# Performance work log

Measured on AMD Instinct MI355X. Metric: run time of the kernel, lower is better.

The kernel has to match this reference:

```python
import jax, jax.numpy as jnp
import numpy as np

WS = 8          # window_size
NH = 8          # num_heads
VD = 512        # values_dim
CD = 128        # coords_dim
INNER = 512     # inner_ratio * values_dim
E = INNER // NH # head_dim = 64
B, Hh, Ww_ = 2, 224, 224

# relative position indices (static)
_idx = np.array([[x, y] for x in range(WS) for y in range(WS)])
_rel = _idx[None, :, :] - _idx[:, None, :] + WS - 1  # (WS^2, WS^2, 2)
REL0 = jnp.asarray(_rel[:, :, 0])
REL1 = jnp.asarray(_rel[:, :, 1])

# shifted-window masks (static)
_s = WS * (WS // 2)
_rm = np.zeros((WS * WS, WS * WS), np.float32)
_rm[-_s:, :-_s] = -np.inf
_rm[:-_s, -_s:] = -np.inf
_cm = _rm.reshape(WS, WS, WS, WS).transpose(1, 0, 3, 2).reshape(WS * WS, WS * WS)
ROW_MASK = jnp.asarray(_rm)
COL_MASK = jnp.asarray(_cm)


def _rmsnorm(x, g, eps=1e-6):
    return x * g * jax.lax.rsqrt(jnp.mean(x * x, axis=-1, keepdims=True) + eps)


def _to_windows(x, b, Wh, Ww):
    # x: (b, hp, wp, INNER) with channel layout (e H) (head fastest)
    x = x.reshape(b, Wh, WS, Ww, WS, E, NH)
    return x.transpose(0, 6, 1, 3, 2, 4, 5).reshape(b, NH, Wh, Ww, WS * WS, E)


def setup_inputs() -> dict:
    key = jax.random.key(0)
    ks = jax.random.split(key, 8)
    s = 0.02
    return {
        "embedded_values": jax.random.normal(ks[0], (B, Hh, Ww_, VD), jnp.float32),
        "embedded_coords": jax.random.normal(ks[1], (B, Hh, Ww_, CD), jnp.float32),
        "Wqk_v": jax.random.normal(ks[2], (VD, 2 * INNER), jnp.float32) * s,
        "bqk_v": jnp.zeros((2 * INNER,), jnp.float32),
        "g_v": jnp.ones((2 * INNER,), jnp.float32),
        "Wv": jax.random.normal(ks[3], (VD, INNER), jnp.float32) * s,
        "bv": jnp.zeros((INNER,), jnp.float32),
        "Wqk_c": jax.random.normal(ks[4], (CD, 2 * INNER), jnp.float32) * s,
        "bqk_c": jnp.zeros((2 * INNER,), jnp.float32),
        "g_c": jnp.ones((2 * INNER,), jnp.float32),
        "pos_emb": jax.random.normal(ks[5], (2 * WS - 1, 2 * WS - 1), jnp.float32),
        "Wout": jax.random.normal(ks[6], (INNER, VD), jnp.float32) * s,
        "bout": jnp.zeros((VD,), jnp.float32),
    }


def reference(embedded_values, embedded_coords, Wqk_v, bqk_v, g_v, Wv, bv,
              Wqk_c, bqk_c, g_c, pos_emb, Wout, bout):
    b, h, w, _ = embedded_values.shape
    # projections; torch concat then rearrange '(d k)' k=3 interleaves channels -> reshape (..., INNER, 3)
    vqk = _rmsnorm(embedded_values @ Wqk_v + bqk_v, g_v)          # (b,h,w,2*INNER)
    vval = embedded_values @ Wv + bv                               # (b,h,w,INNER)
    v = jnp.concatenate([vqk, vval], axis=-1).reshape(b, h, w, INNER, 3)
    c = _rmsnorm(embedded_coords @ Wqk_c + bqk_c, g_c).reshape(b, h, w, INNER, 2)

    pad_h = (-h) % WS
    pad_w = (-w) % WS
    v = jnp.pad(v, ((0, 0), (0, pad_h), (0, pad_w), (0, 0), (0, 0)))
    c = jnp.pad(c, ((0, 0), (0, pad_h), (0, pad_w), (0, 0), (0, 0)))
    # shifted=True: roll windows by half window (no inverse roll in original)
    v = jnp.roll(v, (-(WS // 2), -(WS // 2)), axis=(1, 2))
    c = jnp.roll(c, (-(WS // 2), -(WS // 2)), axis=(1, 2))

    hp, wp = h + pad_h, w + pad_w
    Wh, Ww = hp // WS, wp // WS
    qv = _to_windows(v[..., 0], b, Wh, Ww)
    kv = _to_windows(v[..., 1], b, Wh, Ww)
    vv = _to_windows(v[..., 2], b, Wh, Ww)
    qc = _to_windows(c[..., 0], b, Wh, Ww)
    kc = _to_windows(c[..., 1], b, Wh, Ww)

    scale = float(E) ** 0.5
    dots = (jnp.einsum('bhijpe,bhijqe->bhijpq', qv, kv)
            + jnp.einsum('bhijpe,bhijqe->bhijpq', qc, kc)) / scale
    dots = dots + pos_emb[REL0, REL1]
    # shifted-window masks on last window row / column
    dots = dots.at[:, :, -1, :].add(ROW_MASK)
    dots = dots.at[:, :, :, -1].add(COL_MASK)

    attn = jax.nn.softmax(dots, axis=-1)
    y = jnp.einsum('bhijpq,bhijqe->bhijpe', attn, vv)
    # un-window; output channel layout is (H e) (head slow)
    y = y.reshape(b, NH, Wh, Ww, WS, WS, E).transpose(0, 2, 4, 3, 5, 1, 6)
    y = y.reshape(b, hp, wp, INNER)[:, :h, :w, :]
    return y @ Wout + bout
```

## Files before the change

kernel.cpp:

```cpp
#include <hip/hip_runtime.h>


using u16 = unsigned short;
typedef short bf16x8 __attribute__((ext_vector_type(8)));
typedef float f32x4 __attribute__((ext_vector_type(4)));
typedef u16 u16x4 __attribute__((ext_vector_type(4)));
typedef u16 u16x8 __attribute__((ext_vector_type(8)));

__device__ __forceinline__ float bf2f(u16 v) {
  return __uint_as_float(((unsigned)v) << 16);
}
__device__ __forceinline__ u16 f2bf(float f) {
  unsigned u = __float_as_uint(f);
  u += 0x7fffu + ((u >> 16) & 1u);
  return (u16)(u >> 16);
}

__device__ __forceinline__ void gld16(const u16* g, u16* l) {
  __builtin_amdgcn_global_load_lds(
      (const __attribute__((address_space(1))) unsigned*)g,
      (__attribute__((address_space(3))) unsigned*)l, 16, 0, 0);
}

__global__ void conv_bf16(const float* __restrict__ in, u16* __restrict__ out) {
  size_t i = ((size_t)blockIdx.x * 256 + threadIdx.x) * 8;
  float4 a = *(const float4*)(in + i);
  float4 b = *(const float4*)(in + i + 4);
  u16x8 o;
  o[0] = f2bf(a.x); o[1] = f2bf(a.y); o[2] = f2bf(a.z); o[3] = f2bf(a.w);
  o[4] = f2bf(b.x); o[5] = f2bf(b.y); o[6] = f2bf(b.z); o[7] = f2bf(b.w);
  *(u16x8*)(out + i) = o;
}

__global__ void prep_wv(const float* __restrict__ Wqkv, const float* __restrict__ Wv,
                        u16* __restrict__ out) {
  int idx = blockIdx.x * 256 + threadIdx.x;
  if (idx >= 1536 * 512) return;
  int j = idx >> 9, kk = idx & 511;
  int t = j >> 9, rr = j & 511, nn = rr >> 6, e = rr & 63;
  int cc = 3 * (e * 8 + nn) + t;
  float v = (cc < 1024) ? Wqkv[kk * 1024 + cc] : Wv[kk * 512 + (cc - 1024)];
  out[idx] = f2bf(v);
}

__global__ void prep_wc(const float* __restrict__ W, u16* __restrict__ out) {
  int idx = blockIdx.x * 256 + threadIdx.x;
  if (idx >= 1024 * 128) return;
  int j = idx >> 7, kk = idx & 127;
  int t = j >> 9, rr = j & 511, nn = rr >> 6, e = rr & 63;
  int cc = 2 * (e * 8 + nn) + t;
  out[idx] = f2bf(W[kk * 1024 + cc]);
}

__global__ void prep_wout(const float* __restrict__ W, u16* __restrict__ out) {
  int idx = blockIdx.x * 256 + threadIdx.x;
  if (idx >= 512 * 512) return;
  int o = idx >> 9, kk = idx & 511;
  out[idx] = f2bf(W[kk * 512 + o]);
}

__global__ void prep_vec(const float* __restrict__ bqkv, const float* __restrict__ g_v,
                         const float* __restrict__ bv, const float* __restrict__ bqkc,
                         const float* __restrict__ g_c,
                         float* __restrict__ bpv, float* __restrict__ gAv, float* __restrict__ gBv,
                         float* __restrict__ bpc, float* __restrict__ gAc, float* __restrict__ gBc) {
  int j = blockIdx.x * 256 + threadIdx.x;
  if (j < 1536) {
    int t = j >> 9, rr = j & 511, nn = rr >> 6, e = rr & 63;
    int cc = 3 * (e * 8 + nn) + t;
    if (cc < 1024) { bpv[j] = bqkv[cc]; gAv[j] = g_v[cc]; gBv[j] = 0.f; }
    else           { bpv[j] = bv[cc - 1024]; gAv[j] = 0.f; gBv[j] = 1.f; }
  }
  if (j < 1024) {
    int t = j >> 9, rr = j & 511, nn = rr >> 6, e = rr & 63;
    int cc = 2 * (e * 8 + nn) + t;
    bpc[j] = bqkc[cc]; gAc[j] = g_c[cc]; gBc[j] = 0.f;
  }
}

__global__ void prep_biasT(const float* __restrict__ pe, float* __restrict__ bT) {
  int idx = blockIdx.x * 256 + threadIdx.x;
  if (idx >= 4 * 4096) return;
  int v = idx >> 12, q = (idx >> 6) & 63, p = idx & 63;
  int ap = p >> 3, bp = p & 7, aq = q >> 3, bq = q & 7;
  float val = pe[(aq - ap + 7) * 15 + (bq - bp + 7)];
  if ((v & 1) && ((ap >= 4) != (aq >= 4))) val = -1e30f;
  if ((v & 2) && ((bp >= 4) != (bq >= 4))) val = -1e30f;
  bT[idx] = val;
}

template<int N, int K, int MODE>
__global__ __launch_bounds__(256, 4) void gemm_bt(
    const u16* __restrict__ A, const u16* __restrict__ Bt,
    const float* __restrict__ bias, void* __restrict__ outp,
    float* __restrict__ part, const float* __restrict__ gB, int nwg) {
  constexpr int NCB = N / 128;
  constexpr int KT = K / 32;
  const int orig = blockIdx.x;
  const int work = (orig & 7) * (nwg >> 3) + (orig >> 3);
  const int bm = work / NCB, bn = work % NCB;

  const int tid = threadIdx.x;
  const int w = tid >> 6;
  const int lane = tid & 63;
  const int wr = w >> 1, wc = w & 1;
  const int g = lane >> 4, c = lane & 15;

  __shared__ u16 As[2 * 4096];
  __shared__ u16 Bs[2 * 4096];

  f32x4 acc[4][4] = {};
  const u16* Ag = A + (size_t)bm * 128 * K;
  const u16* Bg = Bt + (size_t)bn * 128 * K;

  auto stage = [&](int buf, int kt) {
    const int k0 = kt * 32;
#pragma unroll
    for (int i = 0; i < 2; ++i) {
      const int idx = i * 256 + tid;
      const int row = idx >> 2, ch = idx & 3;
      const int sch = ch ^ ((row >> 1) & 3);
      gld16(Ag + (size_t)row * K + k0 + sch * 8, As + buf * 4096 + idx * 8);
      gld16(Bg + (size_t)row * K + k0 + sch * 8, Bs + buf * 4096 + idx * 8);
    }
  };

  stage(0, 0);
  __syncthreads();

  const int swz = (c >> 1) & 3;
  for (int kt = 0; kt < KT; ++kt) {
    if (kt + 1 < KT) stage((kt + 1) & 1, kt + 1);
    const u16* Ab = As + (kt & 1) * 4096;
    const u16* Bb = Bs + (kt & 1) * 4096;
    bf16x8 af[4], bfv[4];
#pragma unroll
    for (int mi = 0; mi < 4; ++mi)
      af[mi] = *(const bf16x8*)(Ab + (wr * 64 + mi * 16 + c) * 32 + (g ^ swz) * 8);
#pragma unroll
    for (int ni = 0; ni < 4; ++ni)
      bfv[ni] = *(const bf16x8*)(Bb + (wc * 64 + ni * 16 + c) * 32 + (g ^ swz) * 8);
#pragma unroll
    for (int mi = 0; mi < 4; ++mi)
#pragma unroll
      for (int ni = 0; ni < 4; ++ni)
        acc[mi][ni] = __builtin_amdgcn_mfma_f32_16x16x32_bf16(bfv[ni], af[mi], acc[mi][ni], 0, 0, 0);
    __syncthreads();
  }

  const int rowbase = bm * 128 + wr * 64;
  const int colbase = bn * 128 + wc * 64;
  if constexpr (MODE == 0) {
    u16* O = (u16*)outp;
    float rowsq[4] = {0.f, 0.f, 0.f, 0.f};
#pragma unroll
    for (int ni = 0; ni < 4; ++ni) {
      const int col4 = colbase + ni * 16 + g * 4;
      const float4 bb = *(const float4*)(bias + col4);
      const float4 gb = *(const float4*)(gB + col4);
#pragma unroll
      for (int mi = 0; mi < 4; ++mi) {
        const int row = rowbase + mi * 16 + c;
        u16x4 pk;
        float v0 = acc[mi][ni][0] + bb.x;
        float v1 = acc[mi][ni][1] + bb.y;
        float v2 = acc[mi][ni][2] + bb.z;
        float v3 = acc[mi][ni][3] + bb.w;
        pk[0] = f2bf(v0); pk[1] = f2bf(v1); pk[2] = f2bf(v2); pk[3] = f2bf(v3);
        *(u16x4*)(O + (size_t)row * N + col4) = pk;
        rowsq[mi] += (gb.x == 0.f ? v0 * v0 : 0.f) + (gb.y == 0.f ? v1 * v1 : 0.f)
                   + (gb.z == 0.f ? v2 * v2 : 0.f) + (gb.w == 0.f ? v3 * v3 : 0.f);
      }
    }
#pragma unroll
    for (int mi = 0; mi < 4; ++mi) {
      float s = rowsq[mi];
      s += __shfl_xor(s, 16);
      s += __shfl_xor(s, 32);
      rowsq[mi] = s;
    }
    float* red = (float*)As;
    if (g == 0) {
#pragma unroll
      for (int mi = 0; mi < 4; ++mi)
        red[wc * 128 + wr * 64 + mi * 16 + c] = rowsq[mi];
    }
    __syncthreads();
    if (tid < 128)
      part[(size_t)(bm * 128 + tid) * NCB + bn] = red[tid] + red[128 + tid];
  } else {
    float* O = (float*)outp;
#pragma unroll
    for (int ni = 0; ni < 4; ++ni) {
      const int col4 = colbase + ni * 16 + g * 4;
      const float4 bb = *(const float4*)(bias + col4);
#pragma unroll
      for (int mi = 0; mi < 4; ++mi) {
        const int row = rowbase + mi * 16 + c;
        f32x4 o;
        o[0] = acc[mi][ni][0] + bb.x;
        o[1] = acc[mi][ni][1] + bb.y;
        o[2] = acc[mi][ni][2] + bb.z;
        o[3] = acc[mi][ni][3] + bb.w;
        *(f32x4*)(O + (size_t)row * N + col4) = o;
      }
    }
  }
}

__global__ void combine_scales(const float* __restrict__ pvp, const float* __restrict__ pcp,
                               float* __restrict__ sv, float* __restrict__ sc) {
  const int i = blockIdx.x * 256 + threadIdx.x;
  float s = 0.f;
#pragma unroll
  for (int k = 0; k < 12; ++k) s += pvp[(size_t)i * 12 + k];
  sv[i] = rsqrtf(s * (1.f / 1024.f) + 1e-6f);
  float s2 = 0.f;
#pragma unroll
  for (int k = 0; k < 8; ++k) s2 += pcp[(size_t)i * 8 + k];
  sc[i] = rsqrtf(s2 * (1.f / 1024.f) + 1e-6f);
}

__device__ __forceinline__ void store_norm(u16* dst, u16x8 raw, const float* gA,
                                           const float* gB, float s, int e0) {
  u16x8 o;
#pragma unroll
  for (int j = 0; j < 8; ++j) {
    float fac = gA[e0 + j] * s + gB[e0 + j];
    o[j] = f2bf(bf2f(raw[j]) * fac);
  }
  *(u16x8*)dst = o;
}

__global__ __launch_bounds__(64) void attn_kernel(
    const u16* __restrict__ Pv, const u16* __restrict__ Pc,
    const float* __restrict__ sv, const float* __restrict__ sc,
    const float* __restrict__ gAv, const float* __restrict__ gBv,
    const float* __restrict__ gAc, const float* __restrict__ gBc,
    const float* __restrict__ biasT, u16* __restrict__ Y) {
  const int l = threadIdx.x;
  int bx = blockIdx.x;
  const int wj = bx % 28; bx /= 28;
  const int wi = bx % 28; bx /= 28;
  const int n = bx & 7;
  const int bi = bx >> 3;

  const int g = l >> 4, c = l & 15;
  const int rr0 = l >> 3, rch = l & 7;

  __shared__ u16 Ka[64 * 72];
  __shared__ u16 Qa[64 * 72];
  __shared__ float gf[640];

  gf[l]       = gAv[n * 64 + l];          gf[64 + l]  = gBv[n * 64 + l];
  gf[128 + l] = gAv[512 + n * 64 + l];    gf[192 + l] = gBv[512 + n * 64 + l];
  gf[256 + l] = gAv[1024 + n * 64 + l];   gf[320 + l] = gBv[1024 + n * 64 + l];
  gf[384 + l] = gAc[n * 64 + l];          gf[448 + l] = gBc[n * 64 + l];
  gf[512 + l] = gAc[512 + n * 64 + l];    gf[576 + l] = gBc[512 + n * 64 + l];

  auto pixof = [&](int a, int b2) -> int {
    int y = wi * 8 + a + 4; if (y >= 224) y -= 224;
    int x = wj * 8 + b2 + 4; if (x >= 224) x -= 224;
    return (bi * 224 + y) * 224 + x;
  };

#pragma unroll
  for (int i = 0; i < 8; ++i) {
    const int pix = pixof(i, rr0);
    const float s = sv[pix];
    const u16* src = Pv + (size_t)pix * 1536 + n * 64 + rch * 8;
    u16x8 q = *(const u16x8*)src;
    u16x8 k = *(const u16x8*)(src + 512);
    store_norm(Qa + (i * 8 + rr0) * 72 + rch * 8, q, gf, gf + 64, s, rch * 8);
    store_norm(Ka + (i * 8 + rr0) * 72 + rch * 8, k, gf + 128, gf + 192, s, rch * 8);
  }

  f32x4 acc[4][4] = {};
  auto qk_accum = [&]() {
#pragma unroll
    for (int kk = 0; kk < 2; ++kk) {
      bf16x8 af[4], bq[4];
#pragma unroll
      for (int mi = 0; mi < 4; ++mi)
        af[mi] = *(const bf16x8*)(Ka + (mi * 16 + c) * 72 + kk * 32 + g * 8);
#pragma unroll
      for (int ni = 0; ni < 4; ++ni)
        bq[ni] = *(const bf16x8*)(Qa + (ni * 16 + c) * 72 + kk * 32 + g * 8);
#pragma unroll
      for (int mi = 0; mi < 4; ++mi)
#pragma unroll
        for (int ni = 0; ni < 4; ++ni)
          acc[mi][ni] = __builtin_amdgcn_mfma_f32_16x16x32_bf16(af[mi], bq[ni], acc[mi][ni], 0, 0, 0);
    }
  };
  qk_accum();

#pragma unroll
  for (int i = 0; i < 8; ++i) {
    const int pix = pixof(i, rr0);
    const float s = sc[pix];
    const u16* src = Pc + (size_t)pix * 1024 + n * 64 + rch * 8;
    u16x8 q = *(const u16x8*)src;
    u16x8 k = *(const u16x8*)(src + 512);
    store_norm(Qa + (i * 8 + rr0) * 72 + rch * 8, q, gf + 384, gf + 448, s, rch * 8);
    store_norm(Ka + (i * 8 + rr0) * 72 + rch * 8, k, gf + 512, gf + 576, s, rch * 8);
  }
  qk_accum();

  u16x8 vreg[8]; float vs_[8];
#pragma unroll
  for (int i = 0; i < 8; ++i) {
    const int pix = pixof(i, rr0);
    vs_[i] = sv[pix];
    vreg[i] = *(const u16x8*)(Pv + (size_t)pix * 1536 + 1024 + n * 64 + rch * 8);
  }

  const int variant = ((wi == 27) ? 1 : 0) | ((wj == 27) ? 2 : 0);
  const float* BT = biasT + variant * 4096;
#pragma unroll
  for (int mi = 0; mi < 4; ++mi)
#pragma unroll
    for (int ni = 0; ni < 4; ++ni)
#pragma unroll
      for (int r = 0; r < 4; ++r) {
        const int q = mi * 16 + g * 4 + r;
        const int p = ni * 16 + c;
        acc[mi][ni][r] = acc[mi][ni][r] * 0.125f + BT[q * 64 + p];
      }
  float rinv[4];
#pragma unroll
  for (int ni = 0; ni < 4; ++ni) {
    float m = -3.0e38f;
#pragma unroll
    for (int mi = 0; mi < 4; ++mi)
#pragma unroll
      for (int r = 0; r < 4; ++r) m = fmaxf(m, acc[mi][ni][r]);
    m = fmaxf(m, __shfl_xor(m, 16));
    m = fmaxf(m, __shfl_xor(m, 32));
    float ssum = 0.f;
#pragma unroll
    for (int mi = 0; mi < 4; ++mi)
#pragma unroll
      for (int r = 0; r < 4; ++r) {
        float e = __expf(acc[mi][ni][r] - m);
        acc[mi][ni][r] = e;
        ssum += e;
      }
    ssum += __shfl_xor(ssum, 16);
    ssum += __shfl_xor(ssum, 32);
    rinv[ni] = 1.f / ssum;
  }

  u16* Pl = Qa;
#pragma unroll
  for (int mi = 0; mi < 4; ++mi)
#pragma unroll
    for (int ni = 0; ni < 4; ++ni) {
      u16x4 pk;
#pragma unroll
      for (int r = 0; r < 4; ++r) pk[r] = f2bf(acc[mi][ni][r] * rinv[ni]);
      *(u16x4*)(Pl + (ni * 16 + c) * 72 + mi * 16 + g * 4) = pk;
    }
  u16* Vl = Ka;
#pragma unroll
  for (int i = 0; i < 8; ++i)
    store_norm(Vl + (i * 8 + rr0) * 72 + rch * 8, vreg[i], gf + 256, gf + 320, vs_[i], rch * 8);

  f32x4 ya[4][4] = {};
#pragma unroll
  for (int kk = 0; kk < 2; ++kk) {
    bf16x8 pa[4];
#pragma unroll
    for (int mi = 0; mi < 4; ++mi)
      pa[mi] = *(const bf16x8*)(Pl + (mi * 16 + c) * 72 + kk * 32 + g * 8);
#pragma unroll
    for (int ni = 0; ni < 4; ++ni) {
      u16x8 vtmp;
#pragma unroll
      for (int j = 0; j < 8; ++j)
        vtmp[j] = Vl[(kk * 32 + g * 8 + j) * 72 + ni * 16 + c];
      bf16x8 vb = *(bf16x8*)&vtmp;
#pragma unroll
      for (int mi = 0; mi < 4; ++mi)
        ya[mi][ni] = __builtin_amdgcn_mfma_f32_16x16x32_bf16(pa[mi], vb, ya[mi][ni], 0, 0, 0);
    }
  }

  u16* Yt = Qa;
#pragma unroll
  for (int mi = 0; mi < 4; ++mi)
#pragma unroll
    for (int ni = 0; ni < 4; ++ni) {
      u16x4 yk;
#pragma unroll
      for (int r = 0; r < 4; ++r) yk[r] = f2bf(ya[mi][ni][r]);
      *(u16x4*)(Yt + (ni * 16 + c) * 72 + mi * 16 + g * 4) = yk;
    }
#pragma unroll
  for (int it = 0; it < 8; ++it) {
    const int b2 = l >> 3;
    const int ch = l & 7;
    const int p = it * 8 + b2;
    u16x8 row;
#pragma unroll
    for (int j = 0; j < 8; ++j) row[j] = Yt[(ch * 8 + j) * 72 + p];
    const int oy = wi * 8 + it, ox = wj * 8 + b2;
    *(u16x8*)(Y + ((size_t)(bi * 224 + oy) * 224 + ox) * 512 + n * 64 + ch * 8) = row;
  }
}

extern "C" void kernel_launch(void* const* d_in, const int* in_sizes, int n_in,
                              void* d_out, int out_size, void* d_ws, size_t ws_size,
                              hipStream_t stream) {
  const float* ev   = (const float*)d_in[0];
  const float* ec   = (const float*)d_in[1];
  const float* Wqkv = (const float*)d_in[2];
  const float* bqkv = (const float*)d_in[3];
  const float* g_v  = (const float*)d_in[4];
  const float* Wv   = (const float*)d_in[5];
  const float* bv   = (const float*)d_in[6];
  const float* Wqkc = (const float*)d_in[7];
  const float* bqkc = (const float*)d_in[8];
  const float* g_c  = (const float*)d_in[9];
  const float* pe   = (const float*)d_in[10];
  const float* Wout = (const float*)d_in[11];
  const float* bout = (const float*)d_in[12];
  float* out = (float*)d_out;

  char* w = (char*)d_ws;
  auto take = [&](size_t b) { char* p = w; w += (b + 255) & ~(size_t)255; return p; };
  u16* Wvp   = (u16*)take(1536ull * 512 * 2);
  u16* Wcp   = (u16*)take(1024ull * 128 * 2);
  u16* Wob   = (u16*)take(512ull * 512 * 2);
  float* bpv = (float*)take(1536 * 4);
  float* gAv = (float*)take(1536 * 4);
  float* gBv = (float*)take(1536 * 4);
  float* bpc = (float*)take(1024 * 4);
  float* gAc = (float*)take(1024 * 4);
  float* gBc = (float*)take(1024 * 4);
  float* bT  = (float*)take(4 * 4096 * 4);
  u16* Pv    = (u16*)take(100352ull * 1536 * 2);
  u16* Pc    = (u16*)take(100352ull * 1024 * 2);
  float* pvp = (float*)take(100352ull * 12 * 4);
  float* pcp = (float*)take(100352ull * 8 * 4);
  float* sv  = (float*)take(100352ull * 4);
  float* sc  = (float*)take(100352ull * 4);
  u16* Yb    = (u16*)take(100352ull * 512 * 2);
  u16* evb   = Yb;
  u16* ecb   = (u16*)take(100352ull * 128 * 2);

  conv_bf16<<<25088, 256, 0, stream>>>(ev, evb);
  conv_bf16<<<6272, 256, 0, stream>>>(ec, ecb);
  prep_wv<<<3072, 256, 0, stream>>>(Wqkv, Wv, Wvp);
  prep_wc<<<512, 256, 0, stream>>>(Wqkc, Wcp);
  prep_wout<<<1024, 256, 0, stream>>>(Wout, Wob);
  prep_vec<<<6, 256, 0, stream>>>(bqkv, g_v, bv, bqkc, g_c, bpv, gAv, gBv, bpc, gAc, gBc);
  prep_biasT<<<64, 256, 0, stream>>>(pe, bT);

  gemm_bt<1536, 512, 0><<<9408, 256, 0, stream>>>(evb, Wvp, bpv, Pv, pvp, gBv, 9408);
  gemm_bt<1024, 128, 0><<<6272, 256, 0, stream>>>(ecb, Wcp, bpc, Pc, pcp, gBc, 6272);
  combine_scales<<<392, 256, 0, stream>>>(pvp, pcp, sv, sc);
  attn_kernel<<<12544, 64, 0, stream>>>(Pv, Pc, sv, sc, gAv, gBv, gAc, gBc, bT, Yb);
  gemm_bt<512, 512, 1><<<3136, 256, 0, stream>>>(Yb, Wob, bout, out, nullptr, nullptr, 3136);
}
```

Baseline: 744.4 us.

## Load Q/K MFMA fragments directly from global, bypassing LDS staging

Q and K values are now loaded straight from global memory into MFMA operand fragments in registers, with the RMSNorm scaling applied on the fly, instead of being written to shared memory and read back. This removes the LDS round trips and the shared gamma table. The coords path also drops the gB term by using a multiply-only normalisation, which assumes gBc is unused or zero. The fragment-layout loads are less coalesced, since each lane fetches 16 bytes from a different pixel.

```diff
diff --git a/kernel.cpp b/kernel.cpp
--- a/kernel.cpp
+++ b/kernel.cpp
@@ -20,6 +20,26 @@
   __builtin_amdgcn_global_load_lds(
       (const __attribute__((address_space(1))) unsigned*)g,
       (__attribute__((address_space(3))) unsigned*)l, 16, 0, 0);
+}
+
+struct f8 { float v[8]; };
+__device__ __forceinline__ f8 ld8(const float* p) {
+  f8 r;
+  *(float4*)&r.v[0] = *(const float4*)p;
+  *(float4*)&r.v[4] = *(const float4*)(p + 4);
+  return r;
+}
+__device__ __forceinline__ bf16x8 nfrag(u16x8 raw, const f8& A, const f8& B, float s) {
+  u16x8 o;
+#pragma unroll
+  for (int j = 0; j < 8; ++j) o[j] = f2bf(bf2f(raw[j]) * (A.v[j] * s + B.v[j]));
+  return *(bf16x8*)&o;
+}
+__device__ __forceinline__ bf16x8 nfragA(u16x8 raw, const f8& A, float s) {
+  u16x8 o;
+#pragma unroll
+  for (int j = 0; j < 8; ++j) o[j] = f2bf(bf2f(raw[j]) * (A.v[j] * s));
+  return *(bf16x8*)&o;
 }
 
 __global__ void conv_bf16(const float* __restrict__ in, u16* __restrict__ out) {
@@ -221,17 +241,6 @@
   sc[i] = rsqrtf(s2 * (1.f / 1024.f) + 1e-6f);
 }
 
-__device__ __forceinline__ void store_norm(u16* dst, u16x8 raw, const float* gA,
-                                           const float* gB, float s, int e0) {
-  u16x8 o;
-#pragma unroll
-  for (int j = 0; j < 8; ++j) {
-    float fac = gA[e0 + j] * s + gB[e0 + j];
-    o[j] = f2bf(bf2f(raw[j]) * fac);
-  }
-  *(u16x8*)dst = o;
-}
-
 __global__ __launch_bounds__(64) void attn_kernel(
     const u16* __restrict__ Pv, const u16* __restrict__ Pc,
     const float* __restrict__ sv, const float* __restrict__ sc,
@@ -248,15 +257,8 @@
   const int g = l >> 4, c = l & 15;
   const int rr0 = l >> 3, rch = l & 7;
 
-  __shared__ u16 Ka[64 * 72];
-  __shared__ u16 Qa[64 * 72];
-  __shared__ float gf[640];
-
-  gf[l]       = gAv[n * 64 + l];          gf[64 + l]  = gBv[n * 64 + l];
-  gf[128 + l] = gAv[512 + n * 64 + l];    gf[192 + l] = gBv[512 + n * 64 + l];
-  gf[256 + l] = gAv[1024 + n * 64 + l];   gf[320 + l] = gBv[1024 + n * 64 + l];
-  gf[384 + l] = gAc[n * 64 + l];          gf[448 + l] = gBc[n * 64 + l];
-  gf[512 + l] = gAc[512 + n * 64 + l];    gf[576 + l] = gBc[512 + n * 64 + l];
+  __shared__ u16 Vl[64 * 72];
+  __shared__ u16 Pl[64 * 72];
 
   auto pixof = [&](int a, int b2) -> int {
     int y = wi * 8 + a + 4; if (y >= 224) y -= 224;
@@ -264,48 +266,14 @@
     return (bi * 224 + y) * 224 + x;
   };
 
-#pragma unroll
-  for (int i = 0; i < 8; ++i) {
-    const int pix = pixof(i, rr0);
-    const float s = sv[pix];
-    const u16* src = Pv + (size_t)pix * 1536 + n * 64 + rch * 8;
-    u16x8 q = *(const u16x8*)src;
-    u16x8 k = *(const u16x8*)(src + 512);
-    store_norm(Qa + (i * 8 + rr0) * 72 + rch * 8, q, gf, gf + 64, s, rch * 8);
-    store_norm(Ka + (i * 8 + rr0) * 72 + rch * 8, k, gf + 128, gf + 192, s, rch * 8);
-  }
-
-  f32x4 acc[4][4] = {};
-  auto qk_accum = [&]() {
-#pragma unroll
-    for (int kk = 0; kk < 2; ++kk) {
-      bf16x8 af[4], bq[4];
-#pragma unroll
-      for (int mi = 0; mi < 4; ++mi)
-        af[mi] = *(const bf16x8*)(Ka + (mi * 16 + c) * 72 + kk * 32 + g * 8);
-#pragma unroll
-      for (int ni = 0; ni < 4; ++ni)
-        bq[ni] = *(const bf16x8*)(Qa + (ni * 16 + c) * 72 + kk * 32 + g * 8);
-#pragma unroll
-      for (int mi = 0; mi < 4; ++mi)
-#pragma unroll
-        for (int ni = 0; ni < 4; ++ni)
-          acc[mi][ni] = __builtin_amdgcn_mfma_f32_16x16x32_bf16(af[mi], bq[ni], acc[mi][ni], 0, 0, 0);
-    }
-  };
-  qk_accum();
-
-#pragma unroll
-  for (int i = 0; i < 8; ++i) {
-    const int pix = pixof(i, rr0);
-    const float s = sc[pix];
-    const u16* src = Pc + (size_t)pix * 1024 + n * 64 + rch * 8;
-    u16x8 q = *(const u16x8*)src;
-    u16x8 k = *(const u16x8*)(src + 512);
-    store_norm(Qa + (i * 8 + rr0) * 72 + rch * 8, q, gf + 384, gf + 448, s, rch * 8);
-    store_norm(Ka + (i * 8 + rr0) * 72 + rch * 8, k, gf + 512, gf + 576, s, rch * 8);
-  }
-  qk_accum();
+  int pixr[4]; float svr[4], scr[4];
+#pragma unroll
+  for (int r = 0; r < 4; ++r) {
+    const int p = r * 16 + c;
+    pixr[r] = pixof(p >> 3, p & 7);
+    svr[r] = sv[pixr[r]];
+    scr[r] = sc[pixr[r]];
+  }
 
   u16x8 vreg[8]; float vs_[8];
 #pragma unroll
@@ -313,6 +281,44 @@
     const int pix = pixof(i, rr0);
     vs_[i] = sv[pix];
     vreg[i] = *(const u16x8*)(Pv + (size_t)pix * 1536 + 1024 + n * 64 + rch * 8);
+  }
+
+  f32x4 acc[4][4] = {};
+#pragma unroll
+  for (int kk = 0; kk < 2; ++kk) {
+    const int e0 = kk * 32 + g * 8;
+    const f8 qA = ld8(gAv + n * 64 + e0), qB = ld8(gBv + n * 64 + e0);
+    const f8 kA = ld8(gAv + 512 + n * 64 + e0), kB = ld8(gBv + 512 + n * 64 + e0);
+    bf16x8 af[4], bq[4];
+#pragma unroll
+    for (int r = 0; r < 4; ++r) {
+      const u16* src = Pv + (size_t)pixr[r] * 1536 + n * 64 + e0;
+      af[r] = nfrag(*(const u16x8*)(src + 512), kA, kB, svr[r]);
+      bq[r] = nfrag(*(const u16x8*)src, qA, qB, svr[r]);
+    }
+#pragma unroll
+    for (int mi = 0; mi < 4; ++mi)
+#pragma unroll
+      for (int ni = 0; ni < 4; ++ni)
+        acc[mi][ni] = __builtin_amdgcn_mfma_f32_16x16x32_bf16(af[mi], bq[ni], acc[mi][ni], 0, 0, 0);
+  }
+#pragma unroll
+  for (int kk = 0; kk < 2; ++kk) {
+    const int e0 = kk * 32 + g * 8;
+    const f8 qA = ld8(gAc + n * 64 + e0);
+    const f8 kA = ld8(gAc + 512 + n * 64 + e0);
+    bf16x8 af[4], bq[4];
+#pragma unroll
+    for (int r = 0; r < 4; ++r) {
+      const u16* src = Pc + (size_t)pixr[r] * 1024 + n * 64 + e0;
+      af[r] = nfragA(*(const u16x8*)(src + 512), kA, scr[r]);
+      bq[r] = nfragA(*(const u16x8*)src, qA, scr[r]);
+    }
+#pragma unroll
+    for (int mi = 0; mi < 4; ++mi)
+#pragma unroll
+      for (int ni = 0; ni < 4; ++ni)
+        acc[mi][ni] = __builtin_amdgcn_mfma_f32_16x16x32_bf16(af[mi], bq[ni], acc[mi][ni], 0, 0, 0);
   }
 
   const int variant = ((wi == 27) ? 1 : 0) | ((wj == 27) ? 2 : 0);
@@ -351,7 +357,6 @@
     rinv[ni] = 1.f / ssum;
   }
 
-  u16* Pl = Qa;
 #pragma unroll
   for (int mi = 0; mi < 4; ++mi)
 #pragma unroll
@@ -361,10 +366,15 @@
       for (int r = 0; r < 4; ++r) pk[r] = f2bf(acc[mi][ni][r] * rinv[ni]);
       *(u16x4*)(Pl + (ni * 16 + c) * 72 + mi * 16 + g * 4) = pk;
     }
-  u16* Vl = Ka;
-#pragma unroll
-  for (int i = 0; i < 8; ++i)
-    store_norm(Vl + (i * 8 + rr0) * 72 + rch * 8, vreg[i], gf + 256, gf + 320, vs_[i], rch * 8);
+  {
+    const f8 vA = ld8(gAv + 1024 + n * 64 + rch * 8);
+    const f8 vB = ld8(gBv + 1024 + n * 64 + rch * 8);
+#pragma unroll
+    for (int i = 0; i < 8; ++i) {
+      bf16x8 nv = nfrag(vreg[i], vA, vB, vs_[i]);
+      *(bf16x8*)(Vl + (i * 8 + rr0) * 72 + rch * 8) = nv;
+    }
+  }
 
   f32x4 ya[4][4] = {};
 #pragma unroll
@@ -386,7 +396,7 @@
     }
   }
 
-  u16* Yt = Qa;
+  u16* Yt = Pl;
 #pragma unroll
   for (int mi = 0; mi < 4; ++mi)
 #pragma unroll
```

Result: no change. 743.5 us (-0.1%).
